# Optimization experiments

Hardware: AMD Instinct MI355X
Metric: run time of the kernel (lower is better)

## Reference

```python
import jax, jax.numpy as jnp
import numpy as np

B, S, L = 256, 32, 3            # batch of graph pairs, nodes per graph, num GCN layers
FIN, F = 512, 256               # input feature dim, GCN hidden dim
BIG = 99999.0                   # off-diagonal penalty from the module
EG = 128                        # undirected edges per graph


def _make_edges(rng):
    src = rng.integers(0, S, size=(B, EG))
    dst = rng.integers(0, S, size=(B, EG))
    off = (np.arange(B) * S)[:, None]
    s = (src + off).ravel()
    d = (dst + off).ravel()
    ei = np.stack([np.concatenate([s, d]), np.concatenate([d, s])])  # symmetric
    return jnp.asarray(ei, jnp.int32)


def setup_inputs() -> dict:
    key = jax.random.key(0)
    ks = jax.random.split(key, 8)
    rng = np.random.default_rng(0)
    return {
        "x_q": jax.random.normal(ks[0], (B * S, FIN), jnp.float32),
        "x_c": jax.random.normal(ks[1], (B * S, FIN), jnp.float32),
        "W0": jax.random.normal(ks[2], (FIN, F), jnp.float32) * (FIN ** -0.5),
        "b0": jnp.zeros((F,), jnp.float32),
        "W1": jax.random.normal(ks[3], (F, F), jnp.float32) * (F ** -0.5),
        "b1": jnp.zeros((F,), jnp.float32),
        "W2": jax.random.normal(ks[4], (F, F), jnp.float32) * (F ** -0.5),
        "b2": jnp.zeros((F,), jnp.float32),
        "del_p": jax.random.normal(ks[5], (L, F), jnp.float32) * 0.1,
        "ins_p": jax.random.normal(ks[6], (L, F), jnp.float32) * 0.1,
        "ot_w": jax.random.normal(ks[7], (L,), jnp.float32),
        "ot_b": jnp.zeros((1,), jnp.float32),
        "edge_index_q": _make_edges(rng),
        "edge_index_c": _make_edges(rng),
    }


def _gcn(x, ei, W, b):
    # PyG GCNConv: add self-loops, symmetric deg^-1/2 normalization, then linear
    n = x.shape[0]
    loops = jnp.arange(n, dtype=ei.dtype)
    src = jnp.concatenate([ei[0], loops])
    dst = jnp.concatenate([ei[1], loops])
    deg = jax.ops.segment_sum(jnp.ones(src.shape[0], x.dtype), dst, num_segments=n)
    dinv = jax.lax.rsqrt(deg)
    msg = (x @ W)[src] * (dinv[src] * dinv[dst])[:, None]
    return jax.ops.segment_sum(msg, dst, num_segments=n) + b


def _gnn_feats(x, ei, Ws, bs):
    # features stored pre-ReLU (as in GOTSim.GNN); dropout=0 / eval mode
    feats, h = [], x
    for Wl, bl in zip(Ws, bs):
        h = _gcn(h, ei, Wl, bl)
        feats.append(h)
        h = jax.nn.relu(h)
    return feats


def _sim_matrices(x_q, x_c, W0, b0, W1, b1, W2, b2, del_p, ins_p, ei_q, ei_c):
    Ws, bs = (W0, W1, W2), (b0, b1, b2)
    qf = _gnn_feats(x_q, ei_q, Ws, bs)
    cf = _gnn_feats(x_c, ei_c, Ws, bs)
    eye = jnp.eye(S, dtype=x_q.dtype)
    offd = BIG * (1.0 - eye)
    sims = []
    for i in range(L):
        q = qf[i].reshape(B, S, F)
        c = cf[i].reshape(B, S, F)
        main = -jnp.einsum('bqf,bcf->bqc', q, c)                 # [B,S,S]
        dele = (-(q @ del_p[i]))[:, :, None] * eye + offd        # diag_embed + 99999 offdiag
        ins = (-(c @ ins_p[i]))[:, :, None] * eye + offd
        dummy = jnp.zeros((B, S, S), x_q.dtype)
        sims.append(jnp.concatenate([jnp.concatenate([main, dele], 2),
                                     jnp.concatenate([ins, dummy], 2)], 1))
    return jnp.stack(sims, 1)  # [B, L, 2S, 2S]


def _lap(cost):
    # Jonker-Volgenant shortest augmenting path (same optimum as lapjv);
    # returns col4row: column assigned to each row.
    n = cost.shape[0]
    u = np.zeros(n)
    v = np.zeros(n)
    col4row = np.full(n, -1, np.int64)
    row4col = np.full(n, -1, np.int64)
    for cur in range(n):
        shortest = np.full(n, np.inf)
        path = np.full(n, -1, np.int64)
        SC = np.zeros(n, bool)
        sr_rows = [cur]
        i, min_val, sink = cur, 0.0, -1
        while sink == -1:
            r = min_val + cost[i] - u[i] - v
            upd = (~SC) & (r < shortest)
            shortest[upd] = r[upd]
            path[upd] = i
            masked = np.where(SC, np.inf, shortest)
            j = int(np.argmin(masked))
            min_val = masked[j]
            SC[j] = True
            if row4col[j] < 0:
                sink = j
            else:
                i = int(row4col[j])
                sr_rows.append(i)
        u[cur] += min_val
        for i2 in sr_rows[1:]:
            u[i2] += min_val - shortest[col4row[i2]]
        v[SC] -= min_val - shortest[SC]
        j = sink
        while True:
            i2 = int(path[j])
            row4col[j] = i2
            col4row[i2], j = j, int(col4row[i2])
            if i2 == cur:
                break
    return col4row


def _plans(sim_np):
    # plan[b,l] = eye[col4row] as in dense_wasserstein_distance_v3
    n = sim_np.shape[-1]
    eye = np.eye(n, dtype=np.float32)
    flat = sim_np.reshape(-1, n, n)
    out = np.empty_like(flat, dtype=np.float32)
    for k in range(flat.shape[0]):
        out[k] = eye[_lap(flat[k].astype(np.float64))]
    return out.reshape(sim_np.shape)


def reference(x_q, x_c, W0, b0, W1, b1, W2, b2, del_p, ins_p, ot_w, ot_b,
              edge_index_q, edge_index_c):
    sim = _sim_matrices(x_q, x_c, W0, b0, W1, b1, W2, b2, del_p, ins_p,
                        edge_index_q, edge_index_c)
    plans = jnp.asarray(_plans(np.asarray(sim)))
    mcost = jnp.sum(sim * plans, axis=(2, 3))          # [B, L]
    mcost_norm = 2.0 * mcost / (2.0 * S)               # qsize + csize = 2S
    scores = mcost_norm @ ot_w + ot_b[0]               # Linear(L, 1)
    return jax.nn.sigmoid(scores)                      # is_sig=True -> [B]
```

## Files before the change

### kernel.cpp

```cpp
#include <hip/hip_runtime.h>
#include <math.h>


#define LAP_INF 1e30f

typedef __attribute__((ext_vector_type(8))) short short8;
typedef __attribute__((ext_vector_type(4))) float f32x4;

__device__ __forceinline__ unsigned short bf16_rne(float x) {
  unsigned u = __float_as_uint(x);
  return (unsigned short)((u + 0x7fffu + ((u >> 16) & 1u)) >> 16);
}
__device__ __forceinline__ void split2(float x, unsigned short& h, unsigned short& l) {
  h = bf16_rne(x);
  l = (unsigned short)(__float_as_uint(x - __uint_as_float((unsigned)h << 16)) >> 16);
}

__global__ __launch_bounds__(512) void prep_k(const int* __restrict__ eiq,
                                              const int* __restrict__ eic,
                                              const float* __restrict__ W0,
                                              const float* __restrict__ W1,
                                              const float* __restrict__ W2,
                                              float* __restrict__ adj,
                                              unsigned short* __restrict__ WP,
                                              int ne) {
  const int bx = blockIdx.x;
  const int t = threadIdx.x;
  if (bx < 512) {
    __shared__ float A[1024];
    __shared__ float dinv[32];
    const int g = bx & 255, side = bx >> 8;
    const int* ei = side ? eic : eiq;
    const int half = ne >> 1;
    for (int k = t; k < 1024; k += 512) A[k] = 0.f;
    __syncthreads();
    if (t < 256) {
      int e = (t < 128) ? (g * 128 + t) : (half + g * 128 + (t - 128));
      int s = ei[e];
      int d = ei[ne + e];
      if ((d >> 5) == g)
        atomicAdd(&A[(d & 31) * 32 + (s & 31)], 1.0f);
    }
    __syncthreads();
    if (t < 32) A[t * 32 + t] += 1.0f;
    __syncthreads();
    if (t < 32) {
      float dsum = 0.f;
#pragma unroll
      for (int j = 0; j < 32; ++j) dsum += A[t * 32 + j];
      dinv[t] = rsqrtf(dsum);
    }
    __syncthreads();
    float* dstA = adj + (size_t)(side * 256 + g) * 1024;
    for (int k = t; k < 1024; k += 512)
      dstA[k] = A[k] * dinv[k >> 5] * dinv[k & 31];
  } else {
    __shared__ float tile[32][33];
    int r = bx - 512;
    int z, x, y;
    if (r < 128)      { z = 0; x = r & 15; y = r >> 4; }
    else if (r < 192) { z = 1; r -= 128; x = r & 7; y = r >> 3; }
    else              { z = 2; r -= 192; x = r & 7; y = r >> 3; }
    const float* W = (z == 0) ? W0 : (z == 1) ? W1 : W2;
    const int K = (z == 0) ? 512 : 256;
    unsigned short* WH = WP + ((z == 0) ? 0 : (z == 1) ? 262144 : 393216);
    unsigned short* WL = WH + ((z == 0) ? 131072 : 65536);
    const int k0 = x * 32, n0 = y * 32;
    const int tr = t & 31, tc = t >> 5;
    for (int rr = tc; rr < 32; rr += 16)
      tile[rr][tr] = W[(size_t)(k0 + rr) * 256 + n0 + tr];
    __syncthreads();
    for (int rr = tc; rr < 32; rr += 16) {
      float v = tile[tr][rr];
      unsigned short h, l;
      split2(v, h, l);
      WH[(size_t)(n0 + rr) * K + k0 + tr] = h;
      WL[(size_t)(n0 + rr) * K + k0 + tr] = l;
    }
  }
}

template <int CTRL>
__device__ __forceinline__ float dpp_ror_min(float x) {
  int y = __builtin_amdgcn_update_dpp(0, __float_as_int(x), CTRL, 0xf, 0xf, true);
  return fminf(x, __int_as_float(y));
}
template <int CTRL>
__device__ __forceinline__ float dpp_ror_add(float x) {
  int y = __builtin_amdgcn_update_dpp(0, __float_as_int(x), CTRL, 0xf, 0xf, true);
  return x + __int_as_float(y);
}
__device__ __forceinline__ float rdlane_f(float x, int l) {
  return __int_as_float(__builtin_amdgcn_readlane(__float_as_int(x), l));
}
__device__ __forceinline__ float wave_min32(float x) {
  x = dpp_ror_min<0x121>(x);
  x = dpp_ror_min<0x122>(x);
  x = dpp_ror_min<0x124>(x);
  x = dpp_ror_min<0x128>(x);
  return fminf(rdlane_f(x, 0), rdlane_f(x, 16));
}
#define LDS_FENCE() __asm__ volatile("s_waitcnt lgkmcnt(0)" ::: "memory")

__global__ __launch_bounds__(512, 2) void gnn_k(
    const float* __restrict__ xq, const float* __restrict__ xc,
    const unsigned short* __restrict__ WH0, const unsigned short* __restrict__ WL0,
    const unsigned short* __restrict__ WH1, const unsigned short* __restrict__ WL1,
    const unsigned short* __restrict__ WH2, const unsigned short* __restrict__ WL2,
    const float* __restrict__ adj,
    const float* __restrict__ b0, const float* __restrict__ b1,
    const float* __restrict__ b2,
    const float* __restrict__ delp, const float* __restrict__ insp,
    const float* __restrict__ ot_w, const float* __restrict__ ot_b,
    float* __restrict__ out) {
  __shared__ __align__(16) unsigned short Pp[2][64 * 264];
  __shared__ float Ys[64][258];
  __shared__ float adjs[2048];
  __shared__ __align__(16) float simsbuf[3][1024];
  __shared__ float dq[32], dic[32];
  __shared__ float vlbuf[3][32];
  __shared__ float mc[4];
  unsigned short* SA0 = &Pp[0][0];
  unsigned short* SA1 = &Pp[1][0];

  const int b = blockIdx.x, t = threadIdx.x;
  const int wave = t >> 6, lane = t & 63;
  const int lrow = lane & 15, kgrp = lane >> 4;

  for (int k = t; k < 2048; k += 512)
    adjs[k] = adj[(size_t)((k >> 10) * 256 + b) * 1024 + (k & 1023)];

  for (int l = 0; l < 3; ++l) {
    const unsigned short* WH = (l == 0) ? WH0 : (l == 1) ? WH1 : WH2;
    const unsigned short* WL = (l == 0) ? WL0 : (l == 1) ? WL1 : WL2;
    const float* bias = (l == 0) ? b0 : (l == 1) ? b1 : b2;

    f32x4 acc[4][2];
#pragma unroll
    for (int i = 0; i < 4; ++i)
#pragma unroll
      for (int j = 0; j < 2; ++j) acc[i][j] = (f32x4){0.f, 0.f, 0.f, 0.f};

    if (l == 0) {
      const int arow = t >> 3, aseg = t & 7;
      const float* Asrc = (arow < 32)
          ? (xq + (size_t)(b * 32 + arow) * 512)
          : (xc + (size_t)(b * 32 + (arow - 32)) * 512);
      float4 xv = *(const float4*)(Asrc + aseg * 4);
      short8 pbh[2], pbl[2];
#pragma unroll
      for (int nf = 0; nf < 2; ++nf) {
        const int row = wave * 32 + nf * 16 + lrow;
        pbh[nf] = *(const short8*)&WH[(size_t)row * 512 + kgrp * 8];
        pbl[nf] = *(const short8*)&WL[(size_t)row * 512 + kgrp * 8];
      }
      {
        ushort4 h, lo;
        split2(xv.x, h.x, lo.x); split2(xv.y, h.y, lo.y);
        split2(xv.z, h.z, lo.z); split2(xv.w, h.w, lo.w);
        *(ushort4*)&SA0[arow * 40 + aseg * 4] = h;
        *(ushort4*)&SA1[arow * 40 + aseg * 4] = lo;
      }
      __syncthreads();
      int buf = 0;
      for (int kt = 0; kt < 512; kt += 32) {
        const bool more = (kt + 32 < 512);
        float4 xn;
        if (more) xn = *(const float4*)(Asrc + kt + 32 + aseg * 4);
        short8 bh0 = pbh[0], bh1 = pbh[1];
        short8 bl0 = pbl[0], bl1 = pbl[1];
        if (more) {
#pragma unroll
          for (int nf = 0; nf < 2; ++nf) {
            const int row = wave * 32 + nf * 16 + lrow;
            pbh[nf] = *(const short8*)&WH[(size_t)row * 512 + kt + 32 + kgrp * 8];
            pbl[nf] = *(const short8*)&WL[(size_t)row * 512 + kt + 32 + kgrp * 8];
          }
        }
        short8 ah[4], al[4];
#pragma unroll
        for (int mf = 0; mf < 4; ++mf) {
          const int off = buf * 2560 + (mf * 16 + lrow) * 40 + kgrp * 8;
          ah[mf] = *(const short8*)&SA0[off];
          al[mf] = *(const short8*)&SA1[off];
        }
#pragma unroll
        for (int mf = 0; mf < 4; ++mf) {
          acc[mf][0] = __builtin_amdgcn_mfma_f32_16x16x32_bf16(ah[mf], bh0, acc[mf][0], 0, 0, 0);
          acc[mf][0] = __builtin_amdgcn_mfma_f32_16x16x32_bf16(ah[mf], bl0, acc[mf][0], 0, 0, 0);
          acc[mf][0] = __builtin_amdgcn_mfma_f32_16x16x32_bf16(al[mf], bh0, acc[mf][0], 0, 0, 0);
          acc[mf][1] = __builtin_amdgcn_mfma_f32_16x16x32_bf16(ah[mf], bh1, acc[mf][1], 0, 0, 0);
          acc[mf][1] = __builtin_amdgcn_mfma_f32_16x16x32_bf16(ah[mf], bl1, acc[mf][1], 0, 0, 0);
          acc[mf][1] = __builtin_amdgcn_mfma_f32_16x16x32_bf16(al[mf], bh1, acc[mf][1], 0, 0, 0);
        }
        if (more) {
          ushort4 h, lo;
          split2(xn.x, h.x, lo.x); split2(xn.y, h.y, lo.y);
          split2(xn.z, h.z, lo.z); split2(xn.w, h.w, lo.w);
          *(ushort4*)&SA0[(buf ^ 1) * 2560 + arow * 40 + aseg * 4] = h;
          *(ushort4*)&SA1[(buf ^ 1) * 2560 + arow * 40 + aseg * 4] = lo;
        }
        buf ^= 1;
        __syncthreads();
      }
    } else {
#pragma unroll
      for (int kt8 = 0; kt8 < 8; ++kt8) {
        const int kt = kt8 * 32;
        short8 ah[4], al[4];
#pragma unroll
        for (int mf = 0; mf < 4; ++mf) {
          const int off = (mf * 16 + lrow) * 264 + kt + kgrp * 8;
          ah[mf] = *(const short8*)&Pp[0][off];
          al[mf] = *(const short8*)&Pp[1][off];
        }
#pragma unroll
        for (int nf = 0; nf < 2; ++nf) {
          const int row = wave * 32 + nf * 16 + lrow;
          short8 bh = *(const short8*)&WH[(size_t)row * 256 + kt + kgrp * 8];
          short8 bl = *(const short8*)&WL[(size_t)row * 256 + kt + kgrp * 8];
#pragma unroll
          for (int mf = 0; mf < 4; ++mf) {
            acc[mf][nf] = __builtin_amdgcn_mfma_f32_16x16x32_bf16(ah[mf], bh, acc[mf][nf], 0, 0, 0);
            acc[mf][nf] = __builtin_amdgcn_mfma_f32_16x16x32_bf16(ah[mf], bl, acc[mf][nf], 0, 0, 0);
            acc[mf][nf] = __builtin_amdgcn_mfma_f32_16x16x32_bf16(al[mf], bh, acc[mf][nf], 0, 0, 0);
          }
        }
      }
    }
#pragma unroll
    for (int mf = 0; mf < 4; ++mf)
#pragma unroll
      for (int nf = 0; nf < 2; ++nf)
#pragma unroll
        for (int r = 0; r < 4; ++r)
          Ys[mf * 16 + kgrp * 4 + r][wave * 32 + nf * 16 + lrow] = acc[mf][nf][r];
    __syncthreads();

    const int side = t >> 8, f = t & 255;
    float pv[32];
    {
      const float* A = adjs + side * 1024;
      float y[32];
#pragma unroll
      for (int j = 0; j < 32; ++j) y[j] = Ys[side * 32 + j][f];
      const float bf = bias[f];
#pragma unroll 4
      for (int i = 0; i < 32; ++i) {
        float a = bf;
#pragma unroll
        for (int j = 0; j < 32; ++j) a = fmaf(A[i * 32 + j], y[j], a);
        pv[i] = a;
      }
#pragma unroll
      for (int i = 0; i < 32; ++i) {
        Ys[side * 32 + i][f] = pv[i];
        unsigned short h, lo;
        split2(pv[i], h, lo);
        Pp[0][(side * 32 + i) * 264 + f] = h;
        Pp[1][(side * 32 + i) * 264 + f] = lo;
      }
    }
    __syncthreads();
    {
      const int row = t >> 3, sub = t & 7;
      const float* pvec = ((row < 32) ? delp : insp) + l * 256;
      const float* X = &Ys[row][0];
      float a = 0.f;
#pragma unroll 8
      for (int k = 0; k < 32; ++k) {
        int idx = sub + 8 * k;
        a = fmaf(X[idx], pvec[idx], a);
      }
      a += __shfl_xor(a, 1);
      a += __shfl_xor(a, 2);
      a += __shfl_xor(a, 4);
      if ((t & 7) == 0) { if (row < 32) dq[row] = -a; else dic[row & 31] = -a; }
    }
    __syncthreads();
    if (wave < 4) {
      const int mf = wave >> 1, nf = wave & 1;
      f32x4 sa = (f32x4){0.f, 0.f, 0.f, 0.f};
#pragma unroll
      for (int kt8 = 0; kt8 < 8; ++kt8) {
        const int kt = kt8 * 32;
        const int aoff = (mf * 16 + lrow) * 264 + kt + kgrp * 8;
        const int boff = (32 + nf * 16 + lrow) * 264 + kt + kgrp * 8;
        short8 ah = *(const short8*)&Pp[0][aoff];
        short8 al = *(const short8*)&Pp[1][aoff];
        short8 bh = *(const short8*)&Pp[0][boff];
        short8 bl = *(const short8*)&Pp[1][boff];
        sa = __builtin_amdgcn_mfma_f32_16x16x32_bf16(ah, bh, sa, 0, 0, 0);
        sa = __builtin_amdgcn_mfma_f32_16x16x32_bf16(ah, bl, sa, 0, 0, 0);
        sa = __builtin_amdgcn_mfma_f32_16x16x32_bf16(al, bh, sa, 0, 0, 0);
      }
#pragma unroll
      for (int r = 0; r < 4; ++r) {
        const int m = mf * 16 + kgrp * 4 + r;
        const int n = nf * 16 + lrow;
        simsbuf[l][m * 32 + n] = fminf(-sa[r], dq[m] + dic[n]);
      }
    }
    __syncthreads();
    if (l < 2) {
#pragma unroll
      for (int i = 0; i < 32; ++i) {
        unsigned short h, lo;
        split2(fmaxf(pv[i], 0.f), h, lo);
        Pp[0][(side * 32 + i) * 264 + f] = h;
        Pp[1][(side * 32 + i) * 264 + f] = lo;
      }
      __syncthreads();
    }
  }

  if (wave < 3) {
    if (lane < 32) {
      float* Cl = &simsbuf[wave][0];
      float* vl = &vlbuf[wave][0];
      float minv = LAP_INF;
      int imin = 0;
#pragma unroll
      for (int i = 0; i < 32; ++i) {
        float val = Cl[i * 32 + lane];
        if (val < minv) { minv = val; imin = i; }
      }
      float vj = minv;
      float u = 0.0f;
      int col4row = -1;
      int row4col = -1;
#pragma unroll
      for (int r = 0; r < 32; ++r) {
        unsigned long long bal = __ballot(imin == r);
        if (bal) {
          int j = 63 - __clzll(bal);
          if (lane == j) row4col = r;
          if (lane == r) col4row = j;
        }
      }
      unsigned long long freemask = __ballot(col4row < 0);

      vl[lane] = vj;
      LDS_FENCE();
      {
        float min1 = LAP_INF, min2 = LAP_INF;
        int j1 = -1;
#pragma unroll
        for (int j = 0; j < 32; ++j) {
          float s = Cl[lane * 32 + j] - vl[j];
          if (s < min1) { min2 = min1; min1 = s; j1 = j; }
          else if (s < min2) { min2 = s; }
        }
        float delta = 0.f;
        if (col4row >= 0) {
          delta = (j1 == col4row) ? min2 : min1;
          u = delta;
        }
        int sidx = (row4col < 0) ? lane : row4col;
        float dv = __shfl(delta, sidx);
        if (row4col >= 0) vj -= dv;
      }

      if (freemask) {
        vl[lane] = vj;
        LDS_FENCE();
        float rs = LAP_INF;
#pragma unroll
        for (int j = 0; j < 32; ++j) rs = fminf(rs, Cl[lane * 32 + j] - vl[j]);
        if (col4row < 0) u = rs;
        unsigned long long fm = freemask;
        while (fm) {
          const int r = __ffsll(fm) - 1;
          fm &= fm - 1;
          float m = rdlane_f(rs, r);
          float s = Cl[r * 32 + lane] - vj;
          unsigned long long bal = __ballot((s == m) && (row4col < 0));
          if (bal) {
            int j = __ffsll(bal) - 1;
            if (lane == j) row4col = r;
            if (lane == r) col4row = j;
          }
        }
        freemask = __ballot(col4row < 0);
      }

      while (freemask) {
        const int cur = __ffsll(freemask) - 1;
        freemask &= freemask - 1;
        float shortest = LAP_INF;
        int path = -1;
        bool SC = false;
        int i = cur;
        float minval = 0.0f;
        int sink;
        while (true) {
          float ui = rdlane_f(u, i);
          float r = minval + Cl[i * 32 + lane] - ui - vj;
          bool better = (!SC) && (r < shortest);
          shortest = better ? r : shortest;
          path = better ? i : path;
          float masked = SC ? LAP_INF : shortest;
          float mv = wave_min32(masked);
          unsigned long long bal = __ballot(masked == mv);
          int j = __ffsll(bal) - 1;
          minval = mv;
          SC = SC || (lane == j);
          int rj = __builtin_amdgcn_readlane(row4col, j);
          if (rj < 0) { sink = j; break; }
          i = rj;
        }
        unsigned long long scmask = __ballot(SC);
        if (SC) vj -= minval - shortest;
        int sidx = (col4row < 0) ? lane : col4row;
        float sh_j0 = __shfl(shortest, sidx);
        bool scanned = (col4row >= 0) && ((scmask >> col4row) & 1ull) && (col4row != sink);
        if (lane == cur) u += minval;
        else if (scanned) u += minval - sh_j0;
        int j = sink;
        while (true) {
          int i2 = __builtin_amdgcn_readlane(path, j);
          int jn = __builtin_amdgcn_readlane(col4row, i2);
          if (lane == j) row4col = i2;
          if (lane == i2) col4row = j;
          j = jn;
          if (i2 == cur) break;
        }
      }
      float cc = Cl[lane * 32 + col4row];
      cc = dpp_ror_add<0x121>(cc);
      cc = dpp_ror_add<0x122>(cc);
      cc = dpp_ror_add<0x124>(cc);
      cc = dpp_ror_add<0x128>(cc);
      float tot = rdlane_f(cc, 0) + rdlane_f(cc, 16);
      if (lane == 0) mc[wave] = tot;
    }
  }
  __syncthreads();
  if (t == 0) {
    float s = ot_b[0];
#pragma unroll
    for (int l2 = 0; l2 < 3; ++l2)
      s += mc[l2] * (1.0f / 32.0f) * ot_w[l2];
    out[b] = 1.0f / (1.0f + expf(-s));
  }
}

extern "C" void kernel_launch(void* const* d_in, const int* in_sizes, int n_in,
                              void* d_out, int out_size, void* d_ws, size_t ws_size,
                              hipStream_t stream) {
  const float* x_q  = (const float*)d_in[0];
  const float* x_c  = (const float*)d_in[1];
  const float* W0   = (const float*)d_in[2];
  const float* b0   = (const float*)d_in[3];
  const float* W1   = (const float*)d_in[4];
  const float* b1   = (const float*)d_in[5];
  const float* W2   = (const float*)d_in[6];
  const float* b2   = (const float*)d_in[7];
  const float* delp = (const float*)d_in[8];
  const float* insp = (const float*)d_in[9];
  const float* ot_w = (const float*)d_in[10];
  const float* ot_b = (const float*)d_in[11];
  const int* ei_q   = (const int*)d_in[12];
  const int* ei_c   = (const int*)d_in[13];
  float* out = (float*)d_out;

  float* ws  = (float*)d_ws;
  float* adj = ws;
  unsigned short* WP = (unsigned short*)(adj + 524288);
  unsigned short* WH0 = WP;
  unsigned short* WL0 = WP + 131072;
  unsigned short* WH1 = WP + 262144;
  unsigned short* WL1 = WP + 327680;
  unsigned short* WH2 = WP + 393216;
  unsigned short* WL2 = WP + 458752;

  const int ne = in_sizes[12] / 2;

  prep_k<<<768, 512, 0, stream>>>(ei_q, ei_c, W0, W1, W2, adj, WP, ne);
  gnn_k<<<256, 512, 0, stream>>>(x_q, x_c, WH0, WL0, WH1, WL1, WH2, WL2,
                                 adj, b0, b1, b2, delp, insp, ot_w, ot_b, out);
}
```

Baseline: 169.7 us.

## Split fused GNN kernel into per-side GCN, per-layer sim+LAP, and final kernels

```diff
diff --git a/kernel.cpp b/kernel.cpp
--- a/kernel.cpp
+++ b/kernel.cpp
@@ -14,6 +14,9 @@
 __device__ __forceinline__ void split2(float x, unsigned short& h, unsigned short& l) {
   h = bf16_rne(x);
   l = (unsigned short)(__float_as_uint(x - __uint_as_float((unsigned)h << 16)) >> 16);
+}
+__device__ __forceinline__ float bf2f(unsigned short u) {
+  return __uint_as_float((unsigned)u << 16);
 }
 
 __global__ __launch_bounds__(512) void prep_k(const int* __restrict__ eiq,
@@ -80,29 +83,7 @@
   }
 }
 
-template <int CTRL>
-__device__ __forceinline__ float dpp_ror_min(float x) {
-  int y = __builtin_amdgcn_update_dpp(0, __float_as_int(x), CTRL, 0xf, 0xf, true);
-  return fminf(x, __int_as_float(y));
-}
-template <int CTRL>
-__device__ __forceinline__ float dpp_ror_add(float x) {
-  int y = __builtin_amdgcn_update_dpp(0, __float_as_int(x), CTRL, 0xf, 0xf, true);
-  return x + __int_as_float(y);
-}
-__device__ __forceinline__ float rdlane_f(float x, int l) {
-  return __int_as_float(__builtin_amdgcn_readlane(__float_as_int(x), l));
-}
-__device__ __forceinline__ float wave_min32(float x) {
-  x = dpp_ror_min<0x121>(x);
-  x = dpp_ror_min<0x122>(x);
-  x = dpp_ror_min<0x124>(x);
-  x = dpp_ror_min<0x128>(x);
-  return fminf(rdlane_f(x, 0), rdlane_f(x, 16));
-}
-#define LDS_FENCE() __asm__ volatile("s_waitcnt lgkmcnt(0)" ::: "memory")
-
-__global__ __launch_bounds__(512, 2) void gnn_k(
+__global__ __launch_bounds__(256, 2) void side_k(
     const float* __restrict__ xq, const float* __restrict__ xc,
     const unsigned short* __restrict__ WH0, const unsigned short* __restrict__ WL0,
     const unsigned short* __restrict__ WH1, const unsigned short* __restrict__ WL1,
@@ -111,46 +92,35 @@
     const float* __restrict__ b0, const float* __restrict__ b1,
     const float* __restrict__ b2,
     const float* __restrict__ delp, const float* __restrict__ insp,
-    const float* __restrict__ ot_w, const float* __restrict__ ot_b,
-    float* __restrict__ out) {
-  __shared__ __align__(16) unsigned short Pp[2][64 * 264];
-  __shared__ float Ys[64][258];
-  __shared__ float adjs[2048];
-  __shared__ __align__(16) float simsbuf[3][1024];
-  __shared__ float dq[32], dic[32];
-  __shared__ float vlbuf[3][32];
-  __shared__ float mc[4];
-  unsigned short* SA0 = &Pp[0][0];
-  unsigned short* SA1 = &Pp[1][0];
-
-  const int b = blockIdx.x, t = threadIdx.x;
-  const int wave = t >> 6, lane = t & 63;
-  const int lrow = lane & 15, kgrp = lane >> 4;
-
-  for (int k = t; k < 2048; k += 512)
-    adjs[k] = adj[(size_t)((k >> 10) * 256 + b) * 1024 + (k & 1023)];
+    unsigned int* __restrict__ pg, float* __restrict__ dqg) {
+  __shared__ __align__(16) unsigned short Pp[2][32 * 264];
+  __shared__ float adjs[1024];
+  const int b = blockIdx.x, side = blockIdx.y, t = threadIdx.x;
+  const int wave = t >> 6, lane = t & 63, lrow = lane & 15, kgrp = lane >> 4;
+  unsigned short* SA = &Pp[0][0];
+
+  for (int k = t; k < 1024; k += 256)
+    adjs[k] = adj[(size_t)(side * 256 + b) * 1024 + k];
 
   for (int l = 0; l < 3; ++l) {
     const unsigned short* WH = (l == 0) ? WH0 : (l == 1) ? WH1 : WH2;
     const unsigned short* WL = (l == 0) ? WL0 : (l == 1) ? WL1 : WL2;
     const float* bias = (l == 0) ? b0 : (l == 1) ? b1 : b2;
 
-    f32x4 acc[4][2];
-#pragma unroll
-    for (int i = 0; i < 4; ++i)
-#pragma unroll
-      for (int j = 0; j < 2; ++j) acc[i][j] = (f32x4){0.f, 0.f, 0.f, 0.f};
+    f32x4 acc[2][4];
+#pragma unroll
+    for (int i = 0; i < 2; ++i)
+#pragma unroll
+      for (int j = 0; j < 4; ++j) acc[i][j] = (f32x4){0.f, 0.f, 0.f, 0.f};
 
     if (l == 0) {
       const int arow = t >> 3, aseg = t & 7;
-      const float* Asrc = (arow < 32)
-          ? (xq + (size_t)(b * 32 + arow) * 512)
-          : (xc + (size_t)(b * 32 + (arow - 32)) * 512);
+      const float* Asrc = (side ? xc : xq) + (size_t)(b * 32 + arow) * 512;
       float4 xv = *(const float4*)(Asrc + aseg * 4);
-      short8 pbh[2], pbl[2];
-#pragma unroll
-      for (int nf = 0; nf < 2; ++nf) {
-        const int row = wave * 32 + nf * 16 + lrow;
+      short8 pbh[4], pbl[4];
+#pragma unroll
+      for (int nf = 0; nf < 4; ++nf) {
+        const int row = wave * 64 + nf * 16 + lrow;
         pbh[nf] = *(const short8*)&WH[(size_t)row * 512 + kgrp * 8];
         pbl[nf] = *(const short8*)&WL[(size_t)row * 512 + kgrp * 8];
       }
@@ -158,8 +128,8 @@
         ushort4 h, lo;
         split2(xv.x, h.x, lo.x); split2(xv.y, h.y, lo.y);
         split2(xv.z, h.z, lo.z); split2(xv.w, h.w, lo.w);
-        *(ushort4*)&SA0[arow * 40 + aseg * 4] = h;
-        *(ushort4*)&SA1[arow * 40 + aseg * 4] = lo;
+        *(ushort4*)&SA[arow * 40 + aseg * 4] = h;
+        *(ushort4*)&SA[1280 + arow * 40 + aseg * 4] = lo;
       }
       __syncthreads();
       int buf = 0;
@@ -167,60 +137,60 @@
         const bool more = (kt + 32 < 512);
         float4 xn;
         if (more) xn = *(const float4*)(Asrc + kt + 32 + aseg * 4);
-        short8 bh0 = pbh[0], bh1 = pbh[1];
-        short8 bl0 = pbl[0], bl1 = pbl[1];
+        short8 bh[4], bl[4];
+#pragma unroll
+        for (int nf = 0; nf < 4; ++nf) { bh[nf] = pbh[nf]; bl[nf] = pbl[nf]; }
         if (more) {
 #pragma unroll
-          for (int nf = 0; nf < 2; ++nf) {
-            const int row = wave * 32 + nf * 16 + lrow;
+          for (int nf = 0; nf < 4; ++nf) {
+            const int row = wave * 64 + nf * 16 + lrow;
             pbh[nf] = *(const short8*)&WH[(size_t)row * 512 + kt + 32 + kgrp * 8];
             pbl[nf] = *(const short8*)&WL[(size_t)row * 512 + kt + 32 + kgrp * 8];
           }
         }
-        short8 ah[4], al[4];
-#pragma unroll
-        for (int mf = 0; mf < 4; ++mf) {
+        short8 ah[2], al[2];
+#pragma unroll
+        for (int mf = 0; mf < 2; ++mf) {
           const int off = buf * 2560 + (mf * 16 + lrow) * 40 + kgrp * 8;
-          ah[mf] = *(const short8*)&SA0[off];
-          al[mf] = *(const short8*)&SA1[off];
+          ah[mf] = *(const short8*)&SA[off];
+          al[mf] = *(const short8*)&SA[off + 1280];
         }
 #pragma unroll
-        for (int mf = 0; mf < 4; ++mf) {
-          acc[mf][0] = __builtin_amdgcn_mfma_f32_16x16x32_bf16(ah[mf], bh0, acc[mf][0], 0, 0, 0);
-          acc[mf][0] = __builtin_amdgcn_mfma_f32_16x16x32_bf16(ah[mf], bl0, acc[mf][0], 0, 0, 0);
-          acc[mf][0] = __builtin_amdgcn_mfma_f32_16x16x32_bf16(al[mf], bh0, acc[mf][0], 0, 0, 0);
-          acc[mf][1] = __builtin_amdgcn_mfma_f32_16x16x32_bf16(ah[mf], bh1, acc[mf][1], 0, 0, 0);
-          acc[mf][1] = __builtin_amdgcn_mfma_f32_16x16x32_bf16(ah[mf], bl1, acc[mf][1], 0, 0, 0);
-          acc[mf][1] = __builtin_amdgcn_mfma_f32_16x16x32_bf16(al[mf], bh1, acc[mf][1], 0, 0, 0);
-        }
+        for (int nf = 0; nf < 4; ++nf)
+#pragma unroll
+          for (int mf = 0; mf < 2; ++mf) {
+            acc[mf][nf] = __builtin_amdgcn_mfma_f32_16x16x32_bf16(ah[mf], bh[nf], acc[mf][nf], 0, 0, 0);
+            acc[mf][nf] = __builtin_amdgcn_mfma_f32_16x16x32_bf16(ah[mf], bl[nf], acc[mf][nf], 0, 0, 0);
+            acc[mf][nf] = __builtin_amdgcn_mfma_f32_16x16x32_bf16(al[mf], bh[nf], acc[mf][nf], 0, 0, 0);
+          }
         if (more) {
           ushort4 h, lo;
           split2(xn.x, h.x, lo.x); split2(xn.y, h.y, lo.y);
           split2(xn.z, h.z, lo.z); split2(xn.w, h.w, lo.w);
-          *(ushort4*)&SA0[(buf ^ 1) * 2560 + arow * 40 + aseg * 4] = h;
-          *(ushort4*)&SA1[(buf ^ 1) * 2560 + arow * 40 + aseg * 4] = lo;
+          *(ushort4*)&SA[(buf ^ 1) * 2560 + arow * 40 + aseg * 4] = h;
+          *(ushort4*)&SA[(buf ^ 1) * 2560 + 1280 + arow * 40 + aseg * 4] = lo;
         }
+        __syncthreads();
         buf ^= 1;
-        __syncthreads();
       }
     } else {
 #pragma unroll
       for (int kt8 = 0; kt8 < 8; ++kt8) {
         const int kt = kt8 * 32;
-        short8 ah[4], al[4];
-#pragma unroll
-        for (int mf = 0; mf < 4; ++mf) {
+        short8 ah[2], al[2];
+#pragma unroll
+        for (int mf = 0; mf < 2; ++mf) {
           const int off = (mf * 16 + lrow) * 264 + kt + kgrp * 8;
           ah[mf] = *(const short8*)&Pp[0][off];
           al[mf] = *(const short8*)&Pp[1][off];
         }
 #pragma unroll
-        for (int nf = 0; nf < 2; ++nf) {
-          const int row = wave * 32 + nf * 16 + lrow;
+        for (int nf = 0; nf < 4; ++nf) {
+          const int row = wave * 64 + nf * 16 + lrow;
           short8 bh = *(const short8*)&WH[(size_t)row * 256 + kt + kgrp * 8];
           short8 bl = *(const short8*)&WL[(size_t)row * 256 + kt + kgrp * 8];
 #pragma unroll
-          for (int mf = 0; mf < 4; ++mf) {
+          for (int mf = 0; mf < 2; ++mf) {
             acc[mf][nf] = __builtin_amdgcn_mfma_f32_16x16x32_bf16(ah[mf], bh, acc[mf][nf], 0, 0, 0);
             acc[mf][nf] = __builtin_amdgcn_mfma_f32_16x16x32_bf16(ah[mf], bl, acc[mf][nf], 0, 0, 0);
             acc[mf][nf] = __builtin_amdgcn_mfma_f32_16x16x32_bf16(al[mf], bh, acc[mf][nf], 0, 0, 0);
@@ -228,219 +198,277 @@
         }
       }
     }
-#pragma unroll
-    for (int mf = 0; mf < 4; ++mf)
-#pragma unroll
-      for (int nf = 0; nf < 2; ++nf)
-#pragma unroll
-        for (int r = 0; r < 4; ++r)
-          Ys[mf * 16 + kgrp * 4 + r][wave * 32 + nf * 16 + lrow] = acc[mf][nf][r];
-    __syncthreads();
-
-    const int side = t >> 8, f = t & 255;
+    __syncthreads();
+#pragma unroll
+    for (int mf = 0; mf < 2; ++mf)
+#pragma unroll
+      for (int nf = 0; nf < 4; ++nf)
+#pragma unroll
+        for (int r = 0; r < 4; ++r) {
+          const int row = mf * 16 + kgrp * 4 + r;
+          const int col = wave * 64 + nf * 16 + lrow;
+          unsigned short h, lo;
+          split2(acc[mf][nf][r], h, lo);
+          Pp[0][row * 264 + col] = h;
+          Pp[1][row * 264 + col] = lo;
+        }
+    __syncthreads();
+    const int f = t;
     float pv[32];
     {
-      const float* A = adjs + side * 1024;
       float y[32];
 #pragma unroll
-      for (int j = 0; j < 32; ++j) y[j] = Ys[side * 32 + j][f];
+      for (int j = 0; j < 32; ++j)
+        y[j] = bf2f(Pp[0][j * 264 + f]) + bf2f(Pp[1][j * 264 + f]);
       const float bf = bias[f];
 #pragma unroll 4
       for (int i = 0; i < 32; ++i) {
         float a = bf;
 #pragma unroll
-        for (int j = 0; j < 32; ++j) a = fmaf(A[i * 32 + j], y[j], a);
+        for (int j = 0; j < 32; ++j) a = fmaf(adjs[i * 32 + j], y[j], a);
         pv[i] = a;
       }
-#pragma unroll
-      for (int i = 0; i < 32; ++i) {
-        Ys[side * 32 + i][f] = pv[i];
-        unsigned short h, lo;
-        split2(pv[i], h, lo);
-        Pp[0][(side * 32 + i) * 264 + f] = h;
-        Pp[1][(side * 32 + i) * 264 + f] = lo;
-      }
+    }
+    unsigned int* pgb = pg + ((size_t)(l * 256 + b) * 2 + side) * 8192;
+#pragma unroll
+    for (int i = 0; i < 32; ++i) {
+      unsigned short h, lo;
+      split2(pv[i], h, lo);
+      Pp[0][i * 264 + f] = h;
+      Pp[1][i * 264 + f] = lo;
+      pgb[i * 256 + f] = (unsigned)h | ((unsigned)lo << 16);
     }
     __syncthreads();
     {
       const int row = t >> 3, sub = t & 7;
-      const float* pvec = ((row < 32) ? delp : insp) + l * 256;
-      const float* X = &Ys[row][0];
+      const float* pvec = ((side == 0) ? delp : insp) + l * 256;
       float a = 0.f;
 #pragma unroll 8
       for (int k = 0; k < 32; ++k) {
         int idx = sub + 8 * k;
-        a = fmaf(X[idx], pvec[idx], a);
+        float x = bf2f(Pp[0][row * 264 + idx]) + bf2f(Pp[1][row * 264 + idx]);
+        a = fmaf(x, pvec[idx], a);
       }
       a += __shfl_xor(a, 1);
       a += __shfl_xor(a, 2);
       a += __shfl_xor(a, 4);
-      if ((t & 7) == 0) { if (row < 32) dq[row] = -a; else dic[row & 31] = -a; }
-    }
-    __syncthreads();
-    if (wave < 4) {
-      const int mf = wave >> 1, nf = wave & 1;
-      f32x4 sa = (f32x4){0.f, 0.f, 0.f, 0.f};
-#pragma unroll
-      for (int kt8 = 0; kt8 < 8; ++kt8) {
-        const int kt = kt8 * 32;
-        const int aoff = (mf * 16 + lrow) * 264 + kt + kgrp * 8;
-        const int boff = (32 + nf * 16 + lrow) * 264 + kt + kgrp * 8;
-        short8 ah = *(const short8*)&Pp[0][aoff];
-        short8 al = *(const short8*)&Pp[1][aoff];
-        short8 bh = *(const short8*)&Pp[0][boff];
-        short8 bl = *(const short8*)&Pp[1][boff];
-        sa = __builtin_amdgcn_mfma_f32_16x16x32_bf16(ah, bh, sa, 0, 0, 0);
-        sa = __builtin_amdgcn_mfma_f32_16x16x32_bf16(ah, bl, sa, 0, 0, 0);
-        sa = __builtin_amdgcn_mfma_f32_16x16x32_bf16(al, bh, sa, 0, 0, 0);
-      }
-#pragma unroll
-      for (int r = 0; r < 4; ++r) {
-        const int m = mf * 16 + kgrp * 4 + r;
-        const int n = nf * 16 + lrow;
-        simsbuf[l][m * 32 + n] = fminf(-sa[r], dq[m] + dic[n]);
-      }
-    }
-    __syncthreads();
+      if (sub == 0) dqg[((size_t)(l * 256 + b) * 2 + side) * 32 + row] = -a;
+    }
     if (l < 2) {
+      __syncthreads();
 #pragma unroll
       for (int i = 0; i < 32; ++i) {
         unsigned short h, lo;
         split2(fmaxf(pv[i], 0.f), h, lo);
-        Pp[0][(side * 32 + i) * 264 + f] = h;
-        Pp[1][(side * 32 + i) * 264 + f] = lo;
+        Pp[0][i * 264 + f] = h;
+        Pp[1][i * 264 + f] = lo;
       }
       __syncthreads();
     }
   }
-
-  if (wave < 3) {
-    if (lane < 32) {
-      float* Cl = &simsbuf[wave][0];
-      float* vl = &vlbuf[wave][0];
-      float minv = LAP_INF;
-      int imin = 0;
-#pragma unroll
-      for (int i = 0; i < 32; ++i) {
-        float val = Cl[i * 32 + lane];
-        if (val < minv) { minv = val; imin = i; }
-      }
-      float vj = minv;
-      float u = 0.0f;
-      int col4row = -1;
-      int row4col = -1;
-#pragma unroll
-      for (int r = 0; r < 32; ++r) {
-        unsigned long long bal = __ballot(imin == r);
-        if (bal) {
-          int j = 63 - __clzll(bal);
-          if (lane == j) row4col = r;
-          if (lane == r) col4row = j;
-        }
-      }
-      unsigned long long freemask = __ballot(col4row < 0);
-
-      vl[lane] = vj;
-      LDS_FENCE();
-      {
-        float min1 = LAP_INF, min2 = LAP_INF;
-        int j1 = -1;
-#pragma unroll
-        for (int j = 0; j < 32; ++j) {
-          float s = Cl[lane * 32 + j] - vl[j];
-          if (s < min1) { min2 = min1; min1 = s; j1 = j; }
-          else if (s < min2) { min2 = s; }
-        }
-        float delta = 0.f;
-        if (col4row >= 0) {
-          delta = (j1 == col4row) ? min2 : min1;
-          u = delta;
-        }
-        int sidx = (row4col < 0) ? lane : row4col;
-        float dv = __shfl(delta, sidx);
-        if (row4col >= 0) vj -= dv;
-      }
-
-      if (freemask) {
-        vl[lane] = vj;
-        LDS_FENCE();
-        float rs = LAP_INF;
-#pragma unroll
-        for (int j = 0; j < 32; ++j) rs = fminf(rs, Cl[lane * 32 + j] - vl[j]);
-        if (col4row < 0) u = rs;
-        unsigned long long fm = freemask;
-        while (fm) {
-          const int r = __ffsll(fm) - 1;
-          fm &= fm - 1;
-          float m = rdlane_f(rs, r);
-          float s = Cl[r * 32 + lane] - vj;
-          unsigned long long bal = __ballot((s == m) && (row4col < 0));
-          if (bal) {
-            int j = __ffsll(bal) - 1;
-            if (lane == j) row4col = r;
-            if (lane == r) col4row = j;
-          }
-        }
-        freemask = __ballot(col4row < 0);
-      }
-
-      while (freemask) {
-        const int cur = __ffsll(freemask) - 1;
-        freemask &= freemask - 1;
-        float shortest = LAP_INF;
-        int path = -1;
-        bool SC = false;
-        int i = cur;
-        float minval = 0.0f;
-        int sink;
-        while (true) {
-          float ui = rdlane_f(u, i);
-          float r = minval + Cl[i * 32 + lane] - ui - vj;
-          bool better = (!SC) && (r < shortest);
-          shortest = better ? r : shortest;
-          path = better ? i : path;
-          float masked = SC ? LAP_INF : shortest;
-          float mv = wave_min32(masked);
-          unsigned long long bal = __ballot(masked == mv);
-          int j = __ffsll(bal) - 1;
-          minval = mv;
-          SC = SC || (lane == j);
-          int rj = __builtin_amdgcn_readlane(row4col, j);
-          if (rj < 0) { sink = j; break; }
-          i = rj;
-        }
-        unsigned long long scmask = __ballot(SC);
-        if (SC) vj -= minval - shortest;
-        int sidx = (col4row < 0) ? lane : col4row;
-        float sh_j0 = __shfl(shortest, sidx);
-        bool scanned = (col4row >= 0) && ((scmask >> col4row) & 1ull) && (col4row != sink);
-        if (lane == cur) u += minval;
-        else if (scanned) u += minval - sh_j0;
-        int j = sink;
-        while (true) {
-          int i2 = __builtin_amdgcn_readlane(path, j);
-          int jn = __builtin_amdgcn_readlane(col4row, i2);
-          if (lane == j) row4col = i2;
-          if (lane == i2) col4row = j;
-          j = jn;
-          if (i2 == cur) break;
-        }
-      }
-      float cc = Cl[lane * 32 + col4row];
-      cc = dpp_ror_add<0x121>(cc);
-      cc = dpp_ror_add<0x122>(cc);
-      cc = dpp_ror_add<0x124>(cc);
-      cc = dpp_ror_add<0x128>(cc);
-      float tot = rdlane_f(cc, 0) + rdlane_f(cc, 16);
-      if (lane == 0) mc[wave] = tot;
-    }
+}
+
+template <int CTRL>
+__device__ __forceinline__ float dpp_ror_min(float x) {
+  int y = __builtin_amdgcn_update_dpp(0, __float_as_int(x), CTRL, 0xf, 0xf, true);
+  return fminf(x, __int_as_float(y));
+}
+template <int CTRL>
+__device__ __forceinline__ float dpp_ror_add(float x) {
+  int y = __builtin_amdgcn_update_dpp(0, __float_as_int(x), CTRL, 0xf, 0xf, true);
+  return x + __int_as_float(y);
+}
+__device__ __forceinline__ float rdlane_f(float x, int l) {
+  return __int_as_float(__builtin_amdgcn_readlane(__float_as_int(x), l));
+}
+__device__ __forceinline__ float wave_min32(float x) {
+  x = dpp_ror_min<0x121>(x);
+  x = dpp_ror_min<0x122>(x);
+  x = dpp_ror_min<0x124>(x);
+  x = dpp_ror_min<0x128>(x);
+  return fminf(rdlane_f(x, 0), rdlane_f(x, 16));
+}
+#define LDS_FENCE() __asm__ volatile("s_waitcnt lgkmcnt(0)" ::: "memory")
+
+__device__ __forceinline__ void unpack8(uint4 a, uint4 c, short8& h, short8& l) {
+  h[0] = (short)(a.x & 0xffff); l[0] = (short)(a.x >> 16);
+  h[1] = (short)(a.y & 0xffff); l[1] = (short)(a.y >> 16);
+  h[2] = (short)(a.z & 0xffff); l[2] = (short)(a.z >> 16);
+  h[3] = (short)(a.w & 0xffff); l[3] = (short)(a.w >> 16);
+  h[4] = (short)(c.x & 0xffff); l[4] = (short)(c.x >> 16);
+  h[5] = (short)(c.y & 0xffff); l[5] = (short)(c.y >> 16);
+  h[6] = (short)(c.z & 0xffff); l[6] = (short)(c.z >> 16);
+  h[7] = (short)(c.w & 0xffff); l[7] = (short)(c.w >> 16);
+}
+
+__global__ __launch_bounds__(256) void simlap_k(const unsigned int* __restrict__ pg,
+                                                const float* __restrict__ dqg,
+                                                float* __restrict__ mcost) {
+  __shared__ float Cl[1024];
+  __shared__ float vl[32];
+  __shared__ float dqL[32], dicL[32];
+  const int b = blockIdx.x, l = blockIdx.y;
+  const int t = threadIdx.x, wave = t >> 6, lane = t & 63;
+  const int lrow = lane & 15, kgrp = lane >> 4;
+
+  if (t < 32) dqL[t] = dqg[((size_t)(l * 256 + b) * 2 + 0) * 32 + t];
+  else if (t < 64) dicL[t - 32] = dqg[((size_t)(l * 256 + b) * 2 + 1) * 32 + (t - 32)];
+
+  const unsigned int* qg = pg + ((size_t)(l * 256 + b) * 2 + 0) * 8192;
+  const unsigned int* cg = pg + ((size_t)(l * 256 + b) * 2 + 1) * 8192;
+  const int mf = wave >> 1, nf = wave & 1;
+  f32x4 sa = (f32x4){0.f, 0.f, 0.f, 0.f};
+#pragma unroll
+  for (int kt8 = 0; kt8 < 8; ++kt8) {
+    const int kt = kt8 * 32;
+    const unsigned int* qp = &qg[(mf * 16 + lrow) * 256 + kt + kgrp * 8];
+    const unsigned int* cp = &cg[(nf * 16 + lrow) * 256 + kt + kgrp * 8];
+    uint4 qa = *(const uint4*)qp, qb2 = *(const uint4*)(qp + 4);
+    uint4 ca = *(const uint4*)cp, cb2 = *(const uint4*)(cp + 4);
+    short8 ah, al, bh, bl;
+    unpack8(qa, qb2, ah, al);
+    unpack8(ca, cb2, bh, bl);
+    sa = __builtin_amdgcn_mfma_f32_16x16x32_bf16(ah, bh, sa, 0, 0, 0);
+    sa = __builtin_amdgcn_mfma_f32_16x16x32_bf16(ah, bl, sa, 0, 0, 0);
+    sa = __builtin_amdgcn_mfma_f32_16x16x32_bf16(al, bh, sa, 0, 0, 0);
   }
   __syncthreads();
-  if (t == 0) {
+#pragma unroll
+  for (int r = 0; r < 4; ++r) {
+    const int m = mf * 16 + kgrp * 4 + r;
+    const int n = nf * 16 + lrow;
+    Cl[m * 32 + n] = fminf(-sa[r], dqL[m] + dicL[n]);
+  }
+  __syncthreads();
+  if (wave != 0 || lane >= 32) return;
+
+  float minv = LAP_INF;
+  int imin = 0;
+#pragma unroll
+  for (int i = 0; i < 32; ++i) {
+    float val = Cl[i * 32 + lane];
+    if (val < minv) { minv = val; imin = i; }
+  }
+  float vj = minv;
+  float u = 0.0f;
+  int col4row = -1;
+  int row4col = -1;
+#pragma unroll
+  for (int r = 0; r < 32; ++r) {
+    unsigned long long bal = __ballot(imin == r);
+    if (bal) {
+      int j = 63 - __clzll(bal);
+      if (lane == j) row4col = r;
+      if (lane == r) col4row = j;
+    }
+  }
+  unsigned long long freemask = __ballot(col4row < 0);
+
+  vl[lane] = vj;
+  LDS_FENCE();
+  {
+    float min1 = LAP_INF, min2 = LAP_INF;
+    int j1 = -1;
+#pragma unroll
+    for (int j = 0; j < 32; ++j) {
+      float s = Cl[lane * 32 + j] - vl[j];
+      if (s < min1) { min2 = min1; min1 = s; j1 = j; }
+      else if (s < min2) { min2 = s; }
+    }
+    float delta = 0.f;
+    if (col4row >= 0) {
+      delta = (j1 == col4row) ? min2 : min1;
+      u = delta;
+    }
+    int sidx = (row4col < 0) ? lane : row4col;
+    float dv = __shfl(delta, sidx);
+    if (row4col >= 0) vj -= dv;
+  }
+
+  if (freemask) {
+    vl[lane] = vj;
+    LDS_FENCE();
+    float rs = LAP_INF;
+#pragma unroll
+    for (int j = 0; j < 32; ++j) rs = fminf(rs, Cl[lane * 32 + j] - vl[j]);
+    if (col4row < 0) u = rs;
+    unsigned long long fm = freemask;
+    while (fm) {
+      const int r = __ffsll(fm) - 1;
+      fm &= fm - 1;
+      float m = rdlane_f(rs, r);
+      float s = Cl[r * 32 + lane] - vj;
+      unsigned long long bal = __ballot((s == m) && (row4col < 0));
+      if (bal) {
+        int j = __ffsll(bal) - 1;
+        if (lane == j) row4col = r;
+        if (lane == r) col4row = j;
+      }
+    }
+    freemask = __ballot(col4row < 0);
+  }
+
+  while (freemask) {
+    const int cur = __ffsll(freemask) - 1;
+    freemask &= freemask - 1;
+    float shortest = LAP_INF;
+    int path = -1;
+    bool SC = false;
+    int i = cur;
+    float minval = 0.0f;
+    int sink;
+    while (true) {
+      float ui = rdlane_f(u, i);
+      float r = minval + Cl[i * 32 + lane] - ui - vj;
+      bool better = (!SC) && (r < shortest);
+      shortest = better ? r : shortest;
+      path = better ? i : path;
+      float masked = SC ? LAP_INF : shortest;
+      float mv = wave_min32(masked);
+      unsigned long long bal = __ballot(masked == mv);
+      int j = __ffsll(bal) - 1;
+      minval = mv;
+      SC = SC || (lane == j);
+      int rj = __builtin_amdgcn_readlane(row4col, j);
+      if (rj < 0) { sink = j; break; }
+      i = rj;
+    }
+    unsigned long long scmask = __ballot(SC);
+    if (SC) vj -= minval - shortest;
+    int sidx = (col4row < 0) ? lane : col4row;
+    float sh_j0 = __shfl(shortest, sidx);
+    bool scanned = (col4row >= 0) && ((scmask >> col4row) & 1ull) && (col4row != sink);
+    if (lane == cur) u += minval;
+    else if (scanned) u += minval - sh_j0;
+    int j = sink;
+    while (true) {
+      int i2 = __builtin_amdgcn_readlane(path, j);
+      int jn = __builtin_amdgcn_readlane(col4row, i2);
+      if (lane == j) row4col = i2;
+      if (lane == i2) col4row = j;
+      j = jn;
+      if (i2 == cur) break;
+    }
+  }
+  float cc = Cl[lane * 32 + col4row];
+  cc = dpp_ror_add<0x121>(cc);
+  cc = dpp_ror_add<0x122>(cc);
+  cc = dpp_ror_add<0x124>(cc);
+  cc = dpp_ror_add<0x128>(cc);
+  float tot = rdlane_f(cc, 0) + rdlane_f(cc, 16);
+  if (lane == 0) mcost[b * 3 + l] = tot;
+}
+
+__global__ void final_k(const float* __restrict__ mcost,
+                        const float* __restrict__ ot_w,
+                        const float* __restrict__ ot_b,
+                        float* __restrict__ out) {
+  int b = threadIdx.x;
+  if (b < 256) {
     float s = ot_b[0];
 #pragma unroll
-    for (int l2 = 0; l2 < 3; ++l2)
-      s += mc[l2] * (1.0f / 32.0f) * ot_w[l2];
+    for (int l = 0; l < 3; ++l)
+      s += mcost[b * 3 + l] * (1.0f / 32.0f) * ot_w[l];
     out[b] = 1.0f / (1.0f + expf(-s));
   }
 }
@@ -473,10 +501,16 @@
   unsigned short* WL1 = WP + 327680;
   unsigned short* WH2 = WP + 393216;
   unsigned short* WL2 = WP + 458752;
+  unsigned int* pg = (unsigned int*)(ws + 524288 + 262144);
+  float* dqg = (float*)(pg + 12582912);
+  float* mcost = dqg + 49152;
 
   const int ne = in_sizes[12] / 2;
 
   prep_k<<<768, 512, 0, stream>>>(ei_q, ei_c, W0, W1, W2, adj, WP, ne);
-  gnn_k<<<256, 512, 0, stream>>>(x_q, x_c, WH0, WL0, WH1, WL1, WH2, WL2,
-                                 adj, b0, b1, b2, delp, insp, ot_w, ot_b, out);
-}
+  side_k<<<dim3(256, 2), 256, 0, stream>>>(x_q, x_c, WH0, WL0, WH1, WL1,
+                                           WH2, WL2, adj, b0, b1, b2,
+                                           delp, insp, pg, dqg);
+  simlap_k<<<dim3(256, 3), 256, 0, stream>>>(pg, dqg, mcost);
+  final_k<<<1, 256, 0, stream>>>(mcost, ot_w, ot_b, out);
+}
```

After: 194.4 us. 1.15x slower.

## Run graph aggregation on MFMA with split-bf16 adjacency and transposed activations

Applied to the files above, without the earlier changes.

```diff
diff --git a/kernel.cpp b/kernel.cpp
--- a/kernel.cpp
+++ b/kernel.cpp
@@ -14,6 +14,9 @@
 __device__ __forceinline__ void split2(float x, unsigned short& h, unsigned short& l) {
   h = bf16_rne(x);
   l = (unsigned short)(__float_as_uint(x - __uint_as_float((unsigned)h << 16)) >> 16);
+}
+__device__ __forceinline__ float bf2f(unsigned short u) {
+  return __uint_as_float((unsigned)u << 16);
 }
 
 __global__ __launch_bounds__(512) void prep_k(const int* __restrict__ eiq,
@@ -21,7 +24,8 @@
                                               const float* __restrict__ W0,
                                               const float* __restrict__ W1,
                                               const float* __restrict__ W2,
-                                              float* __restrict__ adj,
+                                              unsigned short* __restrict__ adjPH,
+                                              unsigned short* __restrict__ adjPL,
                                               unsigned short* __restrict__ WP,
                                               int ne) {
   const int bx = blockIdx.x;
@@ -51,9 +55,15 @@
       dinv[t] = rsqrtf(dsum);
     }
     __syncthreads();
-    float* dstA = adj + (size_t)(side * 256 + g) * 1024;
-    for (int k = t; k < 1024; k += 512)
-      dstA[k] = A[k] * dinv[k >> 5] * dinv[k & 31];
+    unsigned short* AH = adjPH + (size_t)(side * 256 + g) * 1024;
+    unsigned short* AL = adjPL + (size_t)(side * 256 + g) * 1024;
+    for (int k = t; k < 1024; k += 512) {
+      float v = A[k] * dinv[k >> 5] * dinv[k & 31];
+      unsigned short h, l;
+      split2(v, h, l);
+      AH[k] = h;
+      AL[k] = l;
+    }
   } else {
     __shared__ float tile[32][33];
     int r = bx - 512;
@@ -107,15 +117,14 @@
     const unsigned short* __restrict__ WH0, const unsigned short* __restrict__ WL0,
     const unsigned short* __restrict__ WH1, const unsigned short* __restrict__ WL1,
     const unsigned short* __restrict__ WH2, const unsigned short* __restrict__ WL2,
-    const float* __restrict__ adj,
+    const unsigned short* __restrict__ adjPH, const unsigned short* __restrict__ adjPL,
     const float* __restrict__ b0, const float* __restrict__ b1,
     const float* __restrict__ b2,
     const float* __restrict__ delp, const float* __restrict__ insp,
     const float* __restrict__ ot_w, const float* __restrict__ ot_b,
     float* __restrict__ out) {
   __shared__ __align__(16) unsigned short Pp[2][64 * 264];
-  __shared__ float Ys[64][258];
-  __shared__ float adjs[2048];
+  __shared__ __align__(16) unsigned short YT[2][256 * 72];
   __shared__ __align__(16) float simsbuf[3][1024];
   __shared__ float dq[32], dic[32];
   __shared__ float vlbuf[3][32];
@@ -126,9 +135,16 @@
   const int b = blockIdx.x, t = threadIdx.x;
   const int wave = t >> 6, lane = t & 63;
   const int lrow = lane & 15, kgrp = lane >> 4;
-
-  for (int k = t; k < 2048; k += 512)
-    adjs[k] = adj[(size_t)((k >> 10) * 256 + b) * 1024 + (k & 1023)];
+  const int aside = wave >> 2;
+  const int wcol = (wave & 3) * 64;
+
+  short8 aAh[2], aAl[2];
+#pragma unroll
+  for (int mf = 0; mf < 2; ++mf) {
+    const size_t base = (size_t)(aside * 256 + b) * 1024 + (mf * 16 + lrow) * 32 + kgrp * 8;
+    aAh[mf] = *(const short8*)&adjPH[base];
+    aAl[mf] = *(const short8*)&adjPL[base];
+  }
 
   for (int l = 0; l < 3; ++l) {
     const unsigned short* WH = (l == 0) ? WH0 : (l == 1) ? WH1 : WH2;
@@ -227,50 +243,71 @@
           }
         }
       }
+      __syncthreads();
     }
 #pragma unroll
     for (int mf = 0; mf < 4; ++mf)
 #pragma unroll
-      for (int nf = 0; nf < 2; ++nf)
-#pragma unroll
-        for (int r = 0; r < 4; ++r)
-          Ys[mf * 16 + kgrp * 4 + r][wave * 32 + nf * 16 + lrow] = acc[mf][nf][r];
-    __syncthreads();
-
-    const int side = t >> 8, f = t & 255;
-    float pv[32];
-    {
-      const float* A = adjs + side * 1024;
-      float y[32];
-#pragma unroll
-      for (int j = 0; j < 32; ++j) y[j] = Ys[side * 32 + j][f];
-      const float bf = bias[f];
-#pragma unroll 4
-      for (int i = 0; i < 32; ++i) {
-        float a = bf;
-#pragma unroll
-        for (int j = 0; j < 32; ++j) a = fmaf(A[i * 32 + j], y[j], a);
-        pv[i] = a;
-      }
-#pragma unroll
-      for (int i = 0; i < 32; ++i) {
-        Ys[side * 32 + i][f] = pv[i];
-        unsigned short h, lo;
-        split2(pv[i], h, lo);
-        Pp[0][(side * 32 + i) * 264 + f] = h;
-        Pp[1][(side * 32 + i) * 264 + f] = lo;
-      }
-    }
+      for (int nf = 0; nf < 2; ++nf) {
+        const int col = wave * 32 + nf * 16 + lrow;
+        ushort4 hv, lv;
+        split2(acc[mf][nf][0], hv.x, lv.x);
+        split2(acc[mf][nf][1], hv.y, lv.y);
+        split2(acc[mf][nf][2], hv.z, lv.z);
+        split2(acc[mf][nf][3], hv.w, lv.w);
+        *(ushort4*)&YT[0][col * 72 + mf * 16 + kgrp * 4] = hv;
+        *(ushort4*)&YT[1][col * 72 + mf * 16 + kgrp * 4] = lv;
+      }
+    __syncthreads();
+
+    f32x4 pacc[2][4];
+    float bv[4];
+#pragma unroll
+    for (int nf = 0; nf < 4; ++nf) {
+      bv[nf] = bias[wcol + nf * 16 + lrow];
+      const int ncol = wcol + nf * 16 + lrow;
+      const int kb = aside * 32 + kgrp * 8;
+      short8 bh = *(const short8*)&YT[0][ncol * 72 + kb];
+      short8 bl = *(const short8*)&YT[1][ncol * 72 + kb];
+#pragma unroll
+      for (int mf = 0; mf < 2; ++mf) {
+        f32x4 pa = (f32x4){0.f, 0.f, 0.f, 0.f};
+        pa = __builtin_amdgcn_mfma_f32_16x16x32_bf16(aAh[mf], bh, pa, 0, 0, 0);
+        pa = __builtin_amdgcn_mfma_f32_16x16x32_bf16(aAh[mf], bl, pa, 0, 0, 0);
+        pa = __builtin_amdgcn_mfma_f32_16x16x32_bf16(aAl[mf], bh, pa, 0, 0, 0);
+        pacc[mf][nf] = pa;
+      }
+    }
+#pragma unroll
+    for (int mf = 0; mf < 2; ++mf)
+#pragma unroll
+      for (int nf = 0; nf < 4; ++nf)
+#pragma unroll
+        for (int r = 0; r < 4; ++r) pacc[mf][nf][r] += bv[nf];
+
+#pragma unroll
+    for (int mf = 0; mf < 2; ++mf)
+#pragma unroll
+      for (int nf = 0; nf < 4; ++nf)
+#pragma unroll
+        for (int r = 0; r < 4; ++r) {
+          const int prow = aside * 32 + mf * 16 + kgrp * 4 + r;
+          const int pcol = wcol + nf * 16 + lrow;
+          unsigned short h, lo;
+          split2(pacc[mf][nf][r], h, lo);
+          Pp[0][prow * 264 + pcol] = h;
+          Pp[1][prow * 264 + pcol] = lo;
+        }
     __syncthreads();
     {
       const int row = t >> 3, sub = t & 7;
       const float* pvec = ((row < 32) ? delp : insp) + l * 256;
-      const float* X = &Ys[row][0];
       float a = 0.f;
 #pragma unroll 8
       for (int k = 0; k < 32; ++k) {
         int idx = sub + 8 * k;
-        a = fmaf(X[idx], pvec[idx], a);
+        float x = bf2f(Pp[0][row * 264 + idx]) + bf2f(Pp[1][row * 264 + idx]);
+        a = fmaf(x, pvec[idx], a);
       }
       a += __shfl_xor(a, 1);
       a += __shfl_xor(a, 2);
@@ -304,12 +341,18 @@
     __syncthreads();
     if (l < 2) {
 #pragma unroll
-      for (int i = 0; i < 32; ++i) {
-        unsigned short h, lo;
-        split2(fmaxf(pv[i], 0.f), h, lo);
-        Pp[0][(side * 32 + i) * 264 + f] = h;
-        Pp[1][(side * 32 + i) * 264 + f] = lo;
-      }
+      for (int mf = 0; mf < 2; ++mf)
+#pragma unroll
+        for (int nf = 0; nf < 4; ++nf)
+#pragma unroll
+          for (int r = 0; r < 4; ++r) {
+            const int prow = aside * 32 + mf * 16 + kgrp * 4 + r;
+            const int pcol = wcol + nf * 16 + lrow;
+            unsigned short h, lo;
+            split2(fmaxf(pacc[mf][nf][r], 0.f), h, lo);
+            Pp[0][prow * 264 + pcol] = h;
+            Pp[1][prow * 264 + pcol] = lo;
+          }
       __syncthreads();
     }
   }
@@ -464,9 +507,9 @@
   const int* ei_c   = (const int*)d_in[13];
   float* out = (float*)d_out;
 
-  float* ws  = (float*)d_ws;
-  float* adj = ws;
-  unsigned short* WP = (unsigned short*)(adj + 524288);
+  unsigned short* adjPH = (unsigned short*)d_ws;
+  unsigned short* adjPL = adjPH + 524288;
+  unsigned short* WP = adjPL + 524288;
   unsigned short* WH0 = WP;
   unsigned short* WL0 = WP + 131072;
   unsigned short* WH1 = WP + 262144;
@@ -476,7 +519,8 @@
 
   const int ne = in_sizes[12] / 2;
 
-  prep_k<<<768, 512, 0, stream>>>(ei_q, ei_c, W0, W1, W2, adj, WP, ne);
+  prep_k<<<768, 512, 0, stream>>>(ei_q, ei_c, W0, W1, W2, adjPH, adjPL, WP, ne);
   gnn_k<<<256, 512, 0, stream>>>(x_q, x_c, WH0, WL0, WH1, WL1, WH2, WL2,
-                                 adj, b0, b1, b2, delp, insp, ot_w, ot_b, out);
-}
+                                 adjPH, adjPL, b0, b1, b2, delp, insp,
+                                 ot_w, ot_b, out);
+}
```

New measurement: 146.8 us. -13.5%, faster.
